# Performance work log

Hardware: AMD Instinct MI355X
Metric: run time of the kernel (lower is better)

## Reference

```python
import jax, jax.numpy as jnp
import numpy as np

HEAD_K_DIM = 128  # linear_key_head_dim (not derivable from weight shapes alone)
EPS_NORM = 1e-6


def _l2norm(x, eps=1e-6):
    return x * jax.lax.rsqrt(jnp.sum(x * x, axis=-1, keepdims=True) + eps)


def setup_inputs() -> dict:
    key = jax.random.key(0)
    ks = jax.random.split(key, 9)
    B, S, H = 2, 1024, 2048
    Hv, Hk, Dk, Dv, K = 32, 16, 128, 128, 4
    key_dim, value_dim = Hk * Dk, Hv * Dv
    C = 2 * key_dim + value_dim  # conv_dim = 8192
    s = 0.02
    return {
        "hidden_states": jax.random.normal(ks[0], (B, S, H), jnp.float32),
        "conv_state": jnp.zeros((B, C, K - 1), jnp.float32),
        "recurrent_state": jnp.zeros((B, Hv, Dk, Dv), jnp.float32),
        "W_qkv": (jax.random.normal(ks[1], (C, H)) * s).astype(jnp.float32),
        "W_z": (jax.random.normal(ks[2], (value_dim, H)) * s).astype(jnp.float32),
        "W_b": (jax.random.normal(ks[3], (Hv, H)) * s).astype(jnp.float32),
        "W_a": (jax.random.normal(ks[4], (Hv, H)) * s).astype(jnp.float32),
        "conv_w": (jax.random.normal(ks[5], (C, K)) * s).astype(jnp.float32),
        "dt_bias": jnp.ones((Hv,), jnp.float32),
        "A_log": jnp.log(jax.random.uniform(ks[6], (Hv,), jnp.float32, 1e-3, 16.0)),
        "norm_weight": jnp.ones((Dv,), jnp.float32),
        "W_out": (jax.random.normal(ks[7], (H, value_dim)) * s).astype(jnp.float32),
    }


def reference(hidden_states, conv_state, recurrent_state, W_qkv, W_z, W_b, W_a,
              conv_w, dt_bias, A_log, norm_weight, W_out):
    B, S, H = hidden_states.shape
    Hv = dt_bias.shape[0]
    Dv = norm_weight.shape[0]
    C, K = conv_w.shape
    value_dim = Hv * Dv
    key_dim = (C - value_dim) // 2
    Dk = HEAD_K_DIM
    Hk = key_dim // Dk

    # input projections
    mixed_qkv = jnp.einsum('bsh,ch->bcs', hidden_states, W_qkv)  # (B, C, S)
    z = hidden_states @ W_z.T                                    # (B, S, value_dim)
    b = hidden_states @ W_b.T                                    # (B, S, Hv)
    a = hidden_states @ W_a.T                                    # (B, S, Hv)

    # causal depthwise conv over time with cached prefix state
    padded = jnp.concatenate([conv_state, mixed_qkv], axis=-1)   # (B, C, K-1+S)
    conv_out = sum(padded[:, :, k:k + S] * conv_w[:, k][None, :, None]
                   for k in range(K))                            # (B, C, S)
    conv_state_new = padded[:, :, -(K - 1):]
    mixed = jnp.swapaxes(jax.nn.silu(conv_out), 1, 2)            # (B, S, C)

    q = mixed[..., :key_dim].reshape(B, S, Hk, Dk)
    k = mixed[..., key_dim:2 * key_dim].reshape(B, S, Hk, Dk)
    v = mixed[..., 2 * key_dim:].reshape(B, S, Hv, Dv)

    beta = jax.nn.sigmoid(b)                                     # (B, S, Hv)
    g = -jnp.exp(A_log) * jax.nn.softplus(a + dt_bias)           # (B, S, Hv)

    rep = Hv // Hk
    if rep > 1:
        q = jnp.repeat(q, rep, axis=2)
        k = jnp.repeat(k, rep, axis=2)

    scale = Dk ** (-0.5)
    q = _l2norm(q) * scale
    k = _l2norm(k)

    # time-leading for scan: (S, B, Hv, ...)
    qT, kT, vT = (jnp.moveaxis(x, 1, 0) for x in (q, k, v))
    gT, betaT = jnp.moveaxis(g, 1, 0), jnp.moveaxis(beta, 1, 0)

    def step(state, xs):
        q_t, k_t, v_t, g_t, beta_t = xs
        state = state * jnp.exp(g_t)[..., None, None]            # decay
        kv_mem = jnp.einsum('bhk,bhkv->bhv', k_t, state)         # read
        delta = (v_t - kv_mem) * beta_t[..., None]               # correction
        state = state + jnp.einsum('bhk,bhv->bhkv', k_t, delta)  # write
        out_t = jnp.einsum('bhk,bhkv->bhv', q_t, state)          # readout
        return state, out_t

    final_state, outs = jax.lax.scan(step, recurrent_state.astype(jnp.float32),
                                     (qT, kT, vT, gT, betaT))
    core = jnp.moveaxis(outs, 0, 1)                              # (B, S, Hv, Dv)

    # gated RMS norm per value head
    var = jnp.mean(core * core, axis=-1, keepdims=True)
    xn = core * jax.lax.rsqrt(var + EPS_NORM) * norm_weight
    gated = xn * jax.nn.silu(z.reshape(B, S, Hv, Dv))

    output = gated.reshape(B, S, value_dim) @ W_out.T            # (B, S, H)
    return output, conv_state_new, final_state
```

## Files before the change

kernel.cpp:

```cpp
#include <hip/hip_runtime.h>
#include <cstdint>
#include <cstddef>

#define B_ 2
#define S_ 1024
#define H_ 2048
#define HV_ 32
#define HK_ 16
#define DK_ 128
#define DV_ 128
#define CC_ 8192
#define KEYDIM_ 2048
#define VALDIM_ 4096
#define NC_ 16
#define CS_ 64
#define NBIG 12416
#define NBIGP 12544

typedef __attribute__((ext_vector_type(8))) short bf16x8;
typedef __attribute__((ext_vector_type(4))) float f32x4;

__device__ __forceinline__ ushort f2bf_rne(float x) {
  union { float f; uint32_t u; } c; c.f = x;
  uint32_t u = c.u + 0x7FFFu + ((c.u >> 16) & 1u);
  return (ushort)(u >> 16);
}

__device__ __forceinline__ void gld16(const void* g, void* l) {
  __builtin_amdgcn_global_load_lds(
      (const __attribute__((address_space(1))) void*)g,
      (__attribute__((address_space(3))) void*)l, 16, 0, 0);
}

__global__ void f2bf_kernel(const float* __restrict__ in, ushort* __restrict__ out, int n) {
  int i = (blockIdx.x * 256 + threadIdx.x) * 4;
  if (i >= n) return;
  float4 v = *(const float4*)(in + i);
  ushort4 o;
  o.x = f2bf_rne(v.x); o.y = f2bf_rne(v.y);
  o.z = f2bf_rne(v.z); o.w = f2bf_rne(v.w);
  *(ushort4*)(out + i) = o;
}

__global__ void wcat_kernel(const float* __restrict__ Wqkv, const float* __restrict__ Wz,
                            const float* __restrict__ Wb, const float* __restrict__ Wa,
                            ushort* __restrict__ out) {
  int i = (blockIdx.x * 256 + threadIdx.x) * 4;
  if (i >= NBIGP * H_) return;
  int n = i >> 11;
  int k = i & (H_ - 1);
  float4 v = make_float4(0.f, 0.f, 0.f, 0.f);
  if (n < 8192)       v = *(const float4*)(Wqkv + (size_t)n * H_ + k);
  else if (n < 12288) v = *(const float4*)(Wz + (size_t)(n - 8192) * H_ + k);
  else if (n < 12320) v = *(const float4*)(Wb + (size_t)(n - 12288) * H_ + k);
  else if (n < 12352) v = *(const float4*)(Wa + (size_t)(n - 12320) * H_ + k);
  ushort4 o;
  o.x = f2bf_rne(v.x); o.y = f2bf_rne(v.y);
  o.z = f2bf_rne(v.z); o.w = f2bf_rne(v.w);
  *(ushort4*)(out + i) = o;
}

#define MEMF() asm volatile("" ::: "memory")
#define VMW(n) asm volatile("s_waitcnt vmcnt(" #n ")" ::: "memory")
#define BARR() do { __builtin_amdgcn_s_barrier(); MEMF(); } while (0)

#define ST(P, SHM, RG, o, kq) do {                                  \
    gld16((P) + (kq),      &SHM[o][((RG) * 2 + 0) * 512]);          \
    gld16((P) + (kq) + 32, &SHM[o][((RG) * 2 + 1) * 512]);          \
  } while (0)

#define LDA(ah, c) do { _Pragma("unroll")                                            \
    for (int i_ = 0; i_ < 4; i_++) { _Pragma("unroll")                               \
      for (int h_ = 0; h_ < 2; h_++)                                                 \
        aF[i_ * 2 + h_] = *(const bf16x8*)(                                          \
            &sAm[c][((wm * 8 + (ah) * 4 + i_) * 2 + h_) * 512 + lane * 8]); } } while (0)

#define LDB(dst, bh, c) do { _Pragma("unroll")                                       \
    for (int j_ = 0; j_ < 2; j_++) { _Pragma("unroll")                               \
      for (int h_ = 0; h_ < 2; h_++)                                                 \
        dst[j_ * 2 + h_] = *(const bf16x8*)(                                         \
            &sBm[c][((wn * 4 + (bh) * 2 + j_) * 2 + h_) * 512 + lane * 8]); } } while (0)

#define MM(ah, bh, bsrc) do {                                                        \
    __builtin_amdgcn_s_setprio(1);                                                   \
    _Pragma("unroll") for (int h_ = 0; h_ < 2; h_++)                                 \
    _Pragma("unroll") for (int i_ = 0; i_ < 4; i_++)                                 \
    _Pragma("unroll") for (int j_ = 0; j_ < 2; j_++)                                 \
      acc[(ah) * 4 + i_][(bh) * 2 + j_] = __builtin_amdgcn_mfma_f32_16x16x32_bf16(   \
          aF[i_ * 2 + h_], bsrc[j_ * 2 + h_], acc[(ah) * 4 + i_][(bh) * 2 + j_],     \
          0, 0, 0);                                                                  \
    __builtin_amdgcn_s_setprio(0);                                                   \
  } while (0)

__global__ __launch_bounds__(512, 2) void gemm256_8ph(
    const ushort* __restrict__ A, const ushort* __restrict__ B,
    float* __restrict__ C, int Ns, int K)
{
  __shared__ ushort sAm[2][16384];
  __shared__ ushort sBm[2][16384];

  const int t = threadIdx.x;
  const int wave = t >> 6, lane = t & 63;
  const int wm = wave >> 2, wn = wave & 3;
  const int l15 = lane & 15, l4 = lane >> 4;
  const int mt = blockIdx.x, nt = blockIdx.y;

  const int rgS0 = (wave & 3) + (wave >> 2) * 8;
  const int rgS3 = rgS0 + 4;
  const int rgS1 = (wave & 1) + (wave >> 1) * 4;
  const int rgS2 = rgS1 + 2;

  const ushort* aP0 = A + (size_t)(mt * 256 + rgS0 * 16 + l15) * K + l4 * 8;
  const ushort* aP1 = A + (size_t)(mt * 256 + rgS3 * 16 + l15) * K + l4 * 8;
  const ushort* bP0 = B + (size_t)(nt * 256 + rgS1 * 16 + l15) * K + l4 * 8;
  const ushort* bP1 = B + (size_t)(nt * 256 + rgS2 * 16 + l15) * K + l4 * 8;

  f32x4 acc[8][4];
  #pragma unroll
  for (int i = 0; i < 8; i++)
    #pragma unroll
    for (int j = 0; j < 4; j++)
      #pragma unroll
      for (int r = 0; r < 4; r++) acc[i][j][r] = 0.f;

  bf16x8 aF[8], bF0[4], bF1[4];

  ST(aP0, sAm, rgS0, 0, 0); MEMF();
  ST(bP0, sBm, rgS1, 0, 0); MEMF();
  ST(bP1, sBm, rgS2, 0, 0); MEMF();
  ST(aP1, sAm, rgS3, 0, 0); MEMF();
  ST(aP0, sAm, rgS0, 1, 64); MEMF();
  VMW(6); BARR();

  const int NT = K >> 6;
  for (int tt = 0; tt < NT; tt++) {
    const int c = tt & 1, o = c ^ 1;
    const int kq1 = (tt + 1 < NT) ? (tt + 1) << 6 : 0;
    const int kq2 = (tt + 2 < NT) ? (tt + 2) << 6 : 0;
    LDA(0, c); LDB(bF0, 0, c);
    VMW(4); BARR();
    ST(bP0, sBm, rgS1, o, kq1); MEMF();
    MM(0, 0, bF0);
    BARR();
    LDB(bF1, 1, c);
    VMW(4); BARR();
    ST(bP1, sBm, rgS2, o, kq1); MEMF();
    MM(0, 1, bF1);
    BARR();
    LDA(1, c);
    VMW(4); BARR();
    ST(aP1, sAm, rgS3, o, kq1); MEMF();
    MM(1, 1, bF1);
    BARR();
    VMW(4); BARR();
    ST(aP0, sAm, rgS0, c, kq2); MEMF();
    MM(1, 0, bF0);
    BARR();
  }
  VMW(0);

  #pragma unroll
  for (int mf = 0; mf < 8; mf++) {
    const int row0 = mt * 256 + wm * 128 + mf * 16 + l4 * 4;
    #pragma unroll
    for (int nf = 0; nf < 4; nf++) {
      const int col = nt * 256 + wn * 64 + nf * 16 + l15;
      if (col < Ns) {
        #pragma unroll
        for (int r = 0; r < 4; r++)
          C[(size_t)(row0 + r) * Ns + col] = acc[mf][nf][r];
      }
    }
  }
}

__device__ __forceinline__ void stage_tile(
    const ushort* aS0, const ushort* aS1, const ushort* bS0, const ushort* bS1,
    ushort* ldsA, ushort* ldsB, int wave, int k0)
{
  #pragma unroll
  for (int h = 0; h < 2; h++) {
    gld16(aS0 + k0 + h * 32, ldsA + h * 4096 + (wave * 2 + 0) * 512);
    gld16(aS1 + k0 + h * 32, ldsA + h * 4096 + (wave * 2 + 1) * 512);
    gld16(bS0 + k0 + h * 32, ldsB + h * 4096 + (wave * 2 + 0) * 512);
    gld16(bS1 + k0 + h * 32, ldsB + h * 4096 + (wave * 2 + 1) * 512);
  }
}

__global__ __launch_bounds__(256) void gemm_bf16_nt(
    const ushort* __restrict__ A, const ushort* __restrict__ B,
    float* __restrict__ C, int M, int N, int K)
{
  __shared__ ushort sL[2][2][8192];
  int t = threadIdx.x;
  int wave = t >> 6, lane = t & 63;
  int wm = wave >> 1, wn = wave & 1;
  int lrow = lane & 15, quad = lane >> 4;
  int mt = blockIdx.x, nt = blockIdx.y;

  f32x4 acc[4][4];
  #pragma unroll
  for (int i = 0; i < 4; i++)
    #pragma unroll
    for (int j = 0; j < 4; j++)
      #pragma unroll
      for (int r = 0; r < 4; r++) acc[i][j][r] = 0.f;

  const ushort* aS0 = A + (size_t)(mt * 128 + (wave * 2 + 0) * 16 + lrow) * K + quad * 8;
  const ushort* aS1 = A + (size_t)(mt * 128 + (wave * 2 + 1) * 16 + lrow) * K + quad * 8;
  const ushort* bS0 = B + (size_t)(nt * 128 + (wave * 2 + 0) * 16 + lrow) * K + quad * 8;
  const ushort* bS1 = B + (size_t)(nt * 128 + (wave * 2 + 1) * 16 + lrow) * K + quad * 8;

  stage_tile(aS0, aS1, bS0, bS1, &sL[0][0][0], &sL[0][1][0], wave, 0);
  __syncthreads();

  const int NK = K >> 6;
  for (int it = 0; it < NK; it++) {
    if (it + 1 < NK)
      stage_tile(aS0, aS1, bS0, bS1,
                 &sL[(it + 1) & 1][0][0], &sL[(it + 1) & 1][1][0],
                 wave, (it + 1) * 64);
    const ushort* bufA = &sL[it & 1][0][0];
    const ushort* bufB = &sL[it & 1][1][0];
    #pragma unroll
    for (int h = 0; h < 2; h++) {
      bf16x8 af[4], bfr[4];
      #pragma unroll
      for (int i = 0; i < 4; i++)
        af[i] = *(const bf16x8*)(bufA + h * 4096 + (wm * 4 + i) * 512 + lane * 8);
      #pragma unroll
      for (int j = 0; j < 4; j++)
        bfr[j] = *(const bf16x8*)(bufB + h * 4096 + (wn * 4 + j) * 512 + lane * 8);
      #pragma unroll
      for (int i = 0; i < 4; i++)
        #pragma unroll
        for (int j = 0; j < 4; j++)
          acc[i][j] = __builtin_amdgcn_mfma_f32_16x16x32_bf16(af[i], bfr[j], acc[i][j], 0, 0, 0);
    }
    __syncthreads();
  }

  #pragma unroll
  for (int i = 0; i < 4; i++) {
    int m_base = mt * 128 + wm * 64 + i * 16 + quad * 4;
    #pragma unroll
    for (int j = 0; j < 4; j++) {
      int n = nt * 128 + wn * 64 + j * 16 + lrow;
      #pragma unroll
      for (int rr = 0; rr < 4; rr++)
        C[(size_t)(m_base + rr) * N + n] = acc[i][j][rr];
    }
  }
}

__global__ void convstate_kernel(const float* __restrict__ Cbig,
                                 float* __restrict__ out)
{
  int idx = blockIdx.x * blockDim.x + threadIdx.x;
  if (idx >= B_ * CC_ * 3) return;
  int j = idx % 3;
  int c = (idx / 3) % CC_;
  int b = idx / (3 * CC_);
  out[idx] = Cbig[((size_t)(b * S_ + (S_ - 3 + j))) * NBIG + c];
}

__global__ __launch_bounds__(128) void prep_qkv(
    const float* __restrict__ Cbig, const float* __restrict__ conv_state,
    const float* __restrict__ conv_w,
    float* __restrict__ Qn, float* __restrict__ Kn, float* __restrict__ Vb)
{
  int group = blockIdx.x, s = blockIdx.y, b = blockIdx.z;
  int t = threadIdx.x;
  int c = group * 128 + t;
  float acc = 0.f;
  #pragma unroll
  for (int kk = 0; kk < 4; kk++) {
    int sp = s - 3 + kk;
    float x = (sp < 0) ? conv_state[((size_t)(b * CC_ + c)) * 3 + (3 + sp)]
                       : Cbig[((size_t)(b * S_ + sp)) * NBIG + c];
    acc += conv_w[c * 4 + kk] * x;
  }
  float val = acc / (1.f + __expf(-acc));

  if (group < 32) {
    __shared__ float red2[2];
    float p = val * val;
    #pragma unroll
    for (int off = 32; off > 0; off >>= 1) p += __shfl_xor(p, off);
    if ((t & 63) == 0) red2[t >> 6] = p;
    __syncthreads();
    float r = rsqrtf(red2[0] + red2[1] + 1e-6f);
    if (group < 16) {
      r *= 0.08838834764831845f;
      Qn[(((size_t)(b * HK_ + group)) * S_ + s) * DK_ + t] = val * r;
    } else {
      Kn[(((size_t)(b * HK_ + (group - 16))) * S_ + s) * DK_ + t] = val * r;
    }
  } else {
    Vb[(((size_t)(b * HV_ + (group - 32))) * S_ + s) * DV_ + t] = val;
  }
}

__global__ void prep_gb(const float* __restrict__ Cbig,
                        const float* __restrict__ A_log, const float* __restrict__ dt_bias,
                        float* __restrict__ g_buf, float* __restrict__ beta_buf)
{
  int idx = blockIdx.x * blockDim.x + threadIdx.x;
  if (idx >= B_ * HV_ * S_) return;
  int s = idx & (S_ - 1);
  int hv = (idx >> 10) & 31;
  int b = idx >> 15;
  float bv = Cbig[((size_t)(b * S_ + s)) * NBIG + 12288 + hv];
  float av = Cbig[((size_t)(b * S_ + s)) * NBIG + 12320 + hv];
  float x = av + dt_bias[hv];
  float sp = (x > 20.f) ? x : log1pf(__expf(x));
  g_buf[idx] = -__expf(A_log[hv]) * sp;
  beta_buf[idx] = 1.f / (1.f + __expf(-bv));
}

__device__ __forceinline__ int swf4(int r, int f) { return r * 32 + (f ^ (r & 31)); }
__device__ __forceinline__ int swf1(int r, int k) {
  return r * 128 + 4 * ((k >> 2) ^ (r & 31)) + (k & 3);
}

__global__ __launch_bounds__(256) void cp_kernel(
    const float* __restrict__ Qn, const float* __restrict__ Kn,
    const float* __restrict__ Vb,
    const float* __restrict__ g_buf, const float* __restrict__ beta_buf,
    float* __restrict__ G_buf, float* __restrict__ M_buf,
    float* __restrict__ KcD, float* __restrict__ D0p)
{
  __shared__ float sK[64 * 128];
  __shared__ float sX[32 * 128];
  __shared__ float sT[64 * 64];
  float* sG  = sT;
  float* sBe = sT + 64;
  float* sA  = sX;
  float* tTw = sX;
  float* tTb = sX;
  float4* sK4 = (float4*)sK;
  float4* sX4 = (float4*)sX;

  const int ch = blockIdx.x;
  const int bh = ch / NC_, c = ch % NC_;
  const int b = bh >> 5, hv = bh & 31, hk = hv >> 1;
  const int s0 = c * CS_;
  const int t = threadIdx.x;
  const size_t gOff = (size_t)bh * S_ + s0;

  float Gw0 = 0.f, Bw0 = 0.f;
  if (t < 64) {
    float gi = g_buf[gOff + t];
    Gw0 = gi;
    #pragma unroll
    for (int off = 1; off < 64; off <<= 1) {
      float o = __shfl_up(Gw0, off);
      if (t >= off) Gw0 += o;
    }
    G_buf[gOff + t] = Gw0;
    sG[t] = Gw0;
    Bw0 = beta_buf[gOff + t];
    sBe[t] = Bw0;
  }
  {
    const float4* src = (const float4*)(Kn + ((size_t)(b * HK_ + hk) * S_ + s0) * DK_);
    #pragma unroll
    for (int u = 0; u < 8; u++) {
      int idx = u * 256 + t;
      sK4[swf4(idx >> 5, idx & 31)] = src[idx];
    }
  }
  __syncthreads();

  const float4* qsrc = (const float4*)(Qn + ((size_t)(b * HK_ + hk) * S_ + s0) * DK_);
  {
    int ti2 = t >> 4, tj = t & 15;
    for (int h = 0; h < 2; h++) {
      #pragma unroll
      for (int u = 0; u < 4; u++) {
        int idx = u * 256 + t;
        sX4[swf4(idx >> 5, idx & 31)] = qsrc[h * 1024 + idx];
      }
      __syncthreads();
      float accM[2][4];
      #pragma unroll
      for (int a = 0; a < 2; a++)
        #pragma unroll
        for (int e = 0; e < 4; e++) accM[a][e] = 0.f;
      for (int k4 = 0; k4 < 32; k4++) {
        float4 qv[2], kv[4];
        qv[0] = sX4[swf4(ti2, k4)];
        qv[1] = sX4[swf4(ti2 + 16, k4)];
        #pragma unroll
        for (int e = 0; e < 4; e++) kv[e] = sK4[swf4(tj + 16 * e, k4)];
        #pragma unroll
        for (int a = 0; a < 2; a++)
          #pragma unroll
          for (int e = 0; e < 4; e++)
            accM[a][e] += qv[a].x * kv[e].x + qv[a].y * kv[e].y +
                          qv[a].z * kv[e].z + qv[a].w * kv[e].w;
      }
      #pragma unroll
      for (int a = 0; a < 2; a++) {
        int iG = h * 32 + ti2 + 16 * a;
        float Gi = sG[iG];
        #pragma unroll
        for (int e = 0; e < 4; e++) {
          int j = tj + 16 * e;
          float m = (j <= iG) ? __expf(Gi - sG[j]) * accM[a][e] : 0.f;
          M_buf[(size_t)ch * 4096 + iG * 64 + j] = m;
        }
      }
      __syncthreads();
    }
  }

  {
    int ti = t >> 4, tj = t & 15;
    float accA[4][4];
    #pragma unroll
    for (int a = 0; a < 4; a++)
      #pragma unroll
      for (int e = 0; e < 4; e++) accA[a][e] = 0.f;
    for (int k4 = 0; k4 < 32; k4++) {
      float4 ki[4], kj[4];
      #pragma unroll
      for (int e = 0; e < 4; e++) {
        ki[e] = sK4[swf4(ti + 16 * e, k4)];
        kj[e] = sK4[swf4(tj + 16 * e, k4)];
      }
      #pragma unroll
      for (int a = 0; a < 4; a++)
        #pragma unroll
        for (int e = 0; e < 4; e++)
          accA[a][e] += ki[a].x * kj[e].x + ki[a].y * kj[e].y +
                        ki[a].z * kj[e].z + ki[a].w * kj[e].w;
    }
    float resA[4][4];
    #pragma unroll
    for (int a = 0; a < 4; a++) {
      int i = ti + 16 * a;
      float Gi = sG[i], Bi = sBe[i];
      #pragma unroll
      for (int e = 0; e < 4; e++) {
        int j = tj + 16 * e;
        resA[a][e] = (j < i) ? Bi * __expf(Gi - sG[j]) * accA[a][e] : 0.f;
      }
    }
    __syncthreads();
    #pragma unroll
    for (int a = 0; a < 4; a++)
      #pragma unroll
      for (int e = 0; e < 4; e++)
        sA[(ti + 16 * a) * 64 + (tj + 16 * e)] = resA[a][e];
  }
  __syncthreads();

  if (t < 64) {
    sT[t] = (t == 0) ? 1.f : 0.f;
    for (int i = 1; i < 64; i++) {
      float acc = 0.f;
      for (int j = 0; j < i; j++) acc += sA[i * 64 + j] * sT[j * 64 + t];
      sT[i * 64 + t] = ((t == i) ? 1.f : 0.f) - acc;
    }
    float w = Bw0 * __expf(Gw0);
    for (int j = 0; j < 64; j++) {
      float wj = __shfl(w, j);
      tTw[j * 64 + t] = sT[t * 64 + j] * wj;
    }
  }
  __syncthreads();

  {
    int i04 = t >> 4, tk = t & 15;
    float accK[4][8];
    #pragma unroll
    for (int r = 0; r < 4; r++)
      #pragma unroll
      for (int u = 0; u < 8; u++) accK[r][u] = 0.f;
    for (int j = 0; j < 64; j++) {
      float4 tw = ((float4*)tTw)[j * 16 + i04];
      #pragma unroll
      for (int u = 0; u < 8; u++) {
        float kv = sK[swf1(j, tk + 16 * u)];
        accK[0][u] += tw.x * kv; accK[1][u] += tw.y * kv;
        accK[2][u] += tw.z * kv; accK[3][u] += tw.w * kv;
      }
    }
    size_t base = (size_t)ch * NBIG;
    #pragma unroll
    for (int r = 0; r < 4; r++)
      #pragma unroll
      for (int u = 0; u < 8; u++)
        KcD[base + (i04 * 4 + r) * 128 + tk + 16 * u] = accK[r][u];
  }
  __syncthreads();

  if (t < 64) {
    for (int j = 0; j < 64; j++) {
      float bj = __shfl(Bw0, j);
      tTb[j * 64 + t] = sT[t * 64 + j] * bj;
    }
  }
  {
    const float4* src = (const float4*)(Vb + ((size_t)bh * S_ + s0) * DV_);
    #pragma unroll
    for (int u = 0; u < 8; u++) {
      int idx = u * 256 + t;
      sK4[swf4(idx >> 5, idx & 31)] = src[idx];
    }
  }
  __syncthreads();

  {
    int i04 = t >> 4, tv_ = t & 15;
    float accD[4][8];
    #pragma unroll
    for (int r = 0; r < 4; r++)
      #pragma unroll
      for (int u = 0; u < 8; u++) accD[r][u] = 0.f;
    for (int j = 0; j < 64; j++) {
      float4 tb = ((float4*)tTb)[j * 16 + i04];
      #pragma unroll
      for (int u = 0; u < 8; u++) {
        float vv = sK[swf1(j, tv_ + 16 * u)];
        accD[0][u] += tb.x * vv; accD[1][u] += tb.y * vv;
        accD[2][u] += tb.z * vv; accD[3][u] += tb.w * vv;
      }
    }
    size_t base = (size_t)ch * NBIG;
    #pragma unroll
    for (int r = 0; r < 4; r++)
      #pragma unroll
      for (int u = 0; u < 8; u++)
        D0p[base + (i04 * 4 + r) * 128 + tv_ + 16 * u] = accD[r][u];
  }
}

__global__ __launch_bounds__(256) void phaseb_kernel(
    const float* __restrict__ rec_state, const float* __restrict__ Qn,
    const float* __restrict__ Kn, const float* __restrict__ G_buf,
    float* __restrict__ KcD, const float* __restrict__ D0p,
    float* __restrict__ Oq_buf, float* __restrict__ final_state)
{
  __shared__ float sS[128 * 32];
  __shared__ float sKT[128 * 64];
  __shared__ float sQT[128 * 64];
  __shared__ float sD[64 * 32];

  const int blk = blockIdx.x;
  const int bh = (blk & 7) | ((blk >> 5) << 3);
  const int vq = (blk >> 3) & 3;
  const int b = bh >> 5, hv = bh & 31, hk = hv >> 1;
  const int t = threadIdx.x;
  const int vbase = vq * 32;
  const float* gG = G_buf + (size_t)bh * S_;

  #pragma unroll
  for (int u = 0; u < 4; u++) {
    int idx = u * 256 + t;
    int k = idx >> 3;
    int v4 = (idx & 7) * 4;
    *(float4*)(&sS[k * 32 + v4]) =
        *(const float4*)(&rec_state[((size_t)bh * 128 + k) * 128 + vbase + v4]);
  }
  __syncthreads();

  const int si = t & 63, skq = t >> 6;
  const int ti = t >> 3;
  const int tv = t & 7;
  const int tk = t >> 3;

  for (int c = 0; c < NC_; c++) {
    const size_t ch = (size_t)bh * NC_ + c;
    const int s0 = c * CS_;
    const float GC = gG[s0 + 63];
    const float eGC = __expf(GC);

    {
      float eGi = __expf(gG[s0 + si]);
      const float* kcRow = KcD + ch * NBIG + si * 128 + skq * 32;
      const float* qRow  = Qn + ((size_t)(b * HK_ + hk) * S_ + s0 + si) * DK_ + skq * 32;
      #pragma unroll
      for (int u = 0; u < 8; u++) {
        float4 kc = *(const float4*)(kcRow + u * 4);
        float4 qv = *(const float4*)(qRow + u * 4);
        int kk = skq * 32 + u * 4;
        sKT[(kk + 0) * 64 + si] = kc.x; sKT[(kk + 1) * 64 + si] = kc.y;
        sKT[(kk + 2) * 64 + si] = kc.z; sKT[(kk + 3) * 64 + si] = kc.w;
        sQT[(kk + 0) * 64 + si] = qv.x * eGi; sQT[(kk + 1) * 64 + si] = qv.y * eGi;
        sQT[(kk + 2) * 64 + si] = qv.z * eGi; sQT[(kk + 3) * 64 + si] = qv.w * eGi;
      }
    }
    __syncthreads();

    {
      float accD[2][4], accO[2][4];
      #pragma unroll
      for (int r = 0; r < 2; r++) {
        float4 d0 = *(const float4*)(&D0p[ch * NBIG + (size_t)(ti * 2 + r) * 128 + vbase + tv * 4]);
        accD[r][0] = d0.x; accD[r][1] = d0.y; accD[r][2] = d0.z; accD[r][3] = d0.w;
        accO[r][0] = accO[r][1] = accO[r][2] = accO[r][3] = 0.f;
      }
      for (int k = 0; k < 128; k++) {
        float2 kc = *(const float2*)(&sKT[k * 64 + ti * 2]);
        float2 qb = *(const float2*)(&sQT[k * 64 + ti * 2]);
        float4 sv = *(const float4*)(&sS[k * 32 + tv * 4]);
        accD[0][0] -= kc.x * sv.x; accD[0][1] -= kc.x * sv.y;
        accD[0][2] -= kc.x * sv.z; accD[0][3] -= kc.x * sv.w;
        accD[1][0] -= kc.y * sv.x; accD[1][1] -= kc.y * sv.y;
        accD[1][2] -= kc.y * sv.z; accD[1][3] -= kc.y * sv.w;
        accO[0][0] += qb.x * sv.x; accO[0][1] += qb.x * sv.y;
        accO[0][2] += qb.x * sv.z; accO[0][3] += qb.x * sv.w;
        accO[1][0] += qb.y * sv.x; accO[1][1] += qb.y * sv.y;
        accO[1][2] += qb.y * sv.z; accO[1][3] += qb.y * sv.w;
      }
      #pragma unroll
      for (int r = 0; r < 2; r++) {
        int i = ti * 2 + r;
        float4 dv = make_float4(accD[r][0], accD[r][1], accD[r][2], accD[r][3]);
        float4 ov = make_float4(accO[r][0], accO[r][1], accO[r][2], accO[r][3]);
        *(float4*)(&sD[i * 32 + tv * 4]) = dv;
        *(float4*)(&KcD[ch * NBIG + (size_t)i * 128 + vbase + tv * 4]) = dv;
        *(float4*)(&Oq_buf[ch * 8192 + (size_t)i * 128 + vbase + tv * 4]) = ov;
      }
    }
    __syncthreads();

    {
      float sc = __expf(GC - gG[s0 + si]);
      const float* kRow = Kn + ((size_t)(b * HK_ + hk) * S_ + s0 + si) * DK_ + skq * 32;
      #pragma unroll
      for (int u = 0; u < 8; u++) {
        float4 x = *(const float4*)(kRow + u * 4);
        x.x *= sc; x.y *= sc; x.z *= sc; x.w *= sc;
        int kg = skq * 8 + u;
        *(float4*)(&sKT[si * 128 + 4 * (kg ^ (si & 31))]) = x;
      }
    }
    __syncthreads();

    {
      float acc[4][4];
      #pragma unroll
      for (int r = 0; r < 4; r++)
        acc[r][0] = acc[r][1] = acc[r][2] = acc[r][3] = 0.f;
      for (int i = 0; i < 64; i++) {
        float4 d  = *(const float4*)(&sD[i * 32 + tv * 4]);
        float4 ka = *(const float4*)(&sKT[i * 128 + 4 * (tk ^ (i & 31))]);
        acc[0][0] += ka.x * d.x; acc[0][1] += ka.x * d.y;
        acc[0][2] += ka.x * d.z; acc[0][3] += ka.x * d.w;
        acc[1][0] += ka.y * d.x; acc[1][1] += ka.y * d.y;
        acc[1][2] += ka.y * d.z; acc[1][3] += ka.y * d.w;
        acc[2][0] += ka.z * d.x; acc[2][1] += ka.z * d.y;
        acc[2][2] += ka.z * d.z; acc[2][3] += ka.z * d.w;
        acc[3][0] += ka.w * d.x; acc[3][1] += ka.w * d.y;
        acc[3][2] += ka.w * d.z; acc[3][3] += ka.w * d.w;
      }
      #pragma unroll
      for (int r = 0; r < 4; r++) {
        int k = tk * 4 + r;
        float4 s = *(const float4*)(&sS[k * 32 + tv * 4]);
        s.x = s.x * eGC + acc[r][0]; s.y = s.y * eGC + acc[r][1];
        s.z = s.z * eGC + acc[r][2]; s.w = s.w * eGC + acc[r][3];
        *(float4*)(&sS[k * 32 + tv * 4]) = s;
      }
    }
    __syncthreads();
  }

  #pragma unroll
  for (int u = 0; u < 4; u++) {
    int idx = u * 256 + t;
    int k = idx >> 3;
    int v4 = (idx & 7) * 4;
    *(float4*)(&final_state[((size_t)bh * 128 + k) * 128 + vbase + v4]) =
        *(const float4*)(&sS[k * 32 + v4]);
  }
}

__global__ __launch_bounds__(128) void phasec_kernel(
    const float* __restrict__ KcD, const float* __restrict__ Oq_buf,
    const float* __restrict__ M_buf, const float* __restrict__ norm_weight,
    const float* __restrict__ Cbig, ushort* __restrict__ zg_bf)
{
  __shared__ float sM[4096];
  __shared__ float red[2][2];
  int ch = blockIdx.x;
  int bh = ch / NC_, c = ch % NC_;
  int b = bh >> 5, hv = bh & 31;
  int s0 = c * CS_;
  int v = threadIdx.x;

  float Dr[64];
  #pragma unroll
  for (int j = 0; j < 64; j++) Dr[j] = KcD[(size_t)ch * NBIG + j * 128 + v];
  {
    const float4* src = (const float4*)(M_buf + (size_t)ch * 4096);
    #pragma unroll
    for (int u = 0; u < 8; u++) ((float4*)sM)[u * 128 + v] = src[u * 128 + v];
  }
  __syncthreads();
  float nw = norm_weight[v];

  for (int i = 0; i < 64; i++) {
    float o = Oq_buf[(size_t)ch * 8192 + i * 128 + v];
    const float4* mr = (const float4*)(sM + i * 64);
    #pragma unroll
    for (int j4 = 0; j4 < 16; j4++) {
      float4 m = mr[j4];
      o += m.x * Dr[4 * j4] + m.y * Dr[4 * j4 + 1] +
           m.z * Dr[4 * j4 + 2] + m.w * Dr[4 * j4 + 3];
    }
    float p = o * o;
    #pragma unroll
    for (int off = 32; off > 0; off >>= 1) p += __shfl_xor(p, off);
    if ((v & 63) == 0) red[i & 1][v >> 6] = p;
    __syncthreads();
    float var = (red[i & 1][0] + red[i & 1][1]) * (1.f / 128.f);
    float xn = o * rsqrtf(var + 1e-6f) * nw;
    float zv = Cbig[((size_t)(b * S_ + s0 + i)) * NBIG + 8192 + hv * DV_ + v];
    zg_bf[((size_t)(b * S_ + s0 + i)) * VALDIM_ + hv * DV_ + v] =
        f2bf_rne(xn * (zv / (1.f + __expf(-zv))));
  }
}

extern "C" void kernel_launch(void* const* d_in, const int* in_sizes, int n_in,
                              void* d_out, int out_size, void* d_ws, size_t ws_size,
                              hipStream_t stream)
{
  const float* hs          = (const float*)d_in[0];
  const float* conv_state  = (const float*)d_in[1];
  const float* rec_state   = (const float*)d_in[2];
  const float* W_qkv       = (const float*)d_in[3];
  const float* W_z         = (const float*)d_in[4];
  const float* W_b         = (const float*)d_in[5];
  const float* W_a         = (const float*)d_in[6];
  const float* conv_w      = (const float*)d_in[7];
  const float* dt_bias     = (const float*)d_in[8];
  const float* A_log       = (const float*)d_in[9];
  const float* norm_weight = (const float*)d_in[10];
  const float* W_out       = (const float*)d_in[11];

  float* out       = (float*)d_out;
  float* out_conv  = out + (size_t)B_ * S_ * H_;
  float* out_state = out_conv + (size_t)B_ * CC_ * 3;

  float* ws = (float*)d_ws;
  float* Cbig = ws;
  float* KcD  = Cbig;
  float* D0p  = Cbig + (size_t)1024 * NBIG;
  float* g_buf    = ws + 25427968;
  float* beta_buf = ws + 25493504;
  float* G_buf    = ws + 25559040;
  float* Qn       = ws + 25624576;
  float* Kn       = ws + 29818880;
  float* Vb       = ws + 34013184;
  float* M_buf    = ws + 42401792;
  float* Oq_buf   = Vb;

  ushort* Wcat_bf = (ushort*)(ws + 25427968);
  ushort* hs_bf   = (ushort*)(ws + 38273024);
  ushort* zg_bf   = (ushort*)Qn;
  ushort* Wout_bf = (ushort*)Kn;

  const int M = B_ * S_;

  f2bf_kernel<<<(M * H_) / 1024, 256, 0, stream>>>(hs, hs_bf, M * H_);
  wcat_kernel<<<(NBIGP * H_) / 1024, 256, 0, stream>>>(W_qkv, W_z, W_b, W_a, Wcat_bf);
  gemm256_8ph<<<dim3(M / 256, NBIGP / 256), 512, 0, stream>>>(hs_bf, Wcat_bf, Cbig, NBIG, H_);
  convstate_kernel<<<(B_ * CC_ * 3 + 255) / 256, 256, 0, stream>>>(Cbig, out_conv);
  prep_qkv<<<dim3(64, S_, B_), 128, 0, stream>>>(Cbig, conv_state, conv_w, Qn, Kn, Vb);
  prep_gb<<<(B_ * HV_ * S_ + 255) / 256, 256, 0, stream>>>(Cbig, A_log, dt_bias, g_buf, beta_buf);
  cp_kernel<<<B_ * HV_ * NC_, 256, 0, stream>>>(Qn, Kn, Vb, g_buf, beta_buf,
                                                G_buf, M_buf, KcD, D0p);
  phaseb_kernel<<<B_ * HV_ * 4, 256, 0, stream>>>(rec_state, Qn, Kn, G_buf,
                                                  KcD, D0p, Oq_buf, out_state);
  f2bf_kernel<<<(H_ * VALDIM_) / 1024, 256, 0, stream>>>(W_out, Wout_bf, H_ * VALDIM_);
  phasec_kernel<<<B_ * HV_ * NC_, 128, 0, stream>>>(KcD, Oq_buf, M_buf,
                                                    norm_weight, Cbig, zg_bf);
  gemm_bf16_nt<<<dim3(M / 128, H_ / 128), 256, 0, stream>>>(zg_bf, Wout_bf, out, M, H_, VALDIM_);
}
```

Baseline: 942.2 us.

## Double phaseb threads with split-K reduction over the recurrent state

Doubles the phase-B block size from 256 to 512 threads. The 128-wide K loop of the chunk output/correction product is split across two thread groups whose partial sums are reduced through a new shared buffer, and the state update gives each thread half as many rows. The sequential scan over chunks runs only 256 blocks, so this aims to shorten per-block latency by adding parallelism per block. The cost is an extra shared-memory reduction and barrier each chunk, more shared memory per block, and idle threads during the reduction.

```diff
diff --git a/kernel.cpp b/kernel.cpp
--- a/kernel.cpp
+++ b/kernel.cpp
@@ -537,7 +537,7 @@
   }
 }
 
-__global__ __launch_bounds__(256) void phaseb_kernel(
+__global__ __launch_bounds__(512) void phaseb_kernel(
     const float* __restrict__ rec_state, const float* __restrict__ Qn,
     const float* __restrict__ Kn, const float* __restrict__ G_buf,
     float* __restrict__ KcD, const float* __restrict__ D0p,
@@ -547,6 +547,7 @@
   __shared__ float sKT[128 * 64];
   __shared__ float sQT[128 * 64];
   __shared__ float sD[64 * 32];
+  __shared__ float sR[2][64 * 32];
 
   const int blk = blockIdx.x;
   const int bh = (blk & 7) | ((blk >> 5) << 3);
@@ -557,8 +558,8 @@
   const float* gG = G_buf + (size_t)bh * S_;
 
   #pragma unroll
-  for (int u = 0; u < 4; u++) {
-    int idx = u * 256 + t;
+  for (int u = 0; u < 2; u++) {
+    int idx = u * 512 + t;
     int k = idx >> 3;
     int v4 = (idx & 7) * 4;
     *(float4*)(&sS[k * 32 + v4]) =
@@ -567,9 +568,10 @@
   __syncthreads();
 
   const int si = t & 63, skq = t >> 6;
-  const int ti = t >> 3;
-  const int tv = t & 7;
-  const int tk = t >> 3;
+  const int kg = t >> 8;
+  const int tt = t & 255;
+  const int ti = tt >> 3, tv = t & 7;
+  const int tp = t >> 3;
 
   for (int c = 0; c < NC_; c++) {
     const size_t ch = (size_t)bh * NC_ + c;
@@ -579,13 +581,13 @@
 
     {
       float eGi = __expf(gG[s0 + si]);
-      const float* kcRow = KcD + ch * NBIG + si * 128 + skq * 32;
-      const float* qRow  = Qn + ((size_t)(b * HK_ + hk) * S_ + s0 + si) * DK_ + skq * 32;
-      #pragma unroll
-      for (int u = 0; u < 8; u++) {
+      const float* kcRow = KcD + ch * NBIG + si * 128 + skq * 16;
+      const float* qRow  = Qn + ((size_t)(b * HK_ + hk) * S_ + s0 + si) * DK_ + skq * 16;
+      #pragma unroll
+      for (int u = 0; u < 4; u++) {
         float4 kc = *(const float4*)(kcRow + u * 4);
         float4 qv = *(const float4*)(qRow + u * 4);
-        int kk = skq * 32 + u * 4;
+        int kk = skq * 16 + u * 4;
         sKT[(kk + 0) * 64 + si] = kc.x; sKT[(kk + 1) * 64 + si] = kc.y;
         sKT[(kk + 2) * 64 + si] = kc.z; sKT[(kk + 3) * 64 + si] = kc.w;
         sQT[(kk + 0) * 64 + si] = qv.x * eGi; sQT[(kk + 1) * 64 + si] = qv.y * eGi;
@@ -598,11 +600,18 @@
       float accD[2][4], accO[2][4];
       #pragma unroll
       for (int r = 0; r < 2; r++) {
-        float4 d0 = *(const float4*)(&D0p[ch * NBIG + (size_t)(ti * 2 + r) * 128 + vbase + tv * 4]);
-        accD[r][0] = d0.x; accD[r][1] = d0.y; accD[r][2] = d0.z; accD[r][3] = d0.w;
         accO[r][0] = accO[r][1] = accO[r][2] = accO[r][3] = 0.f;
-      }
-      for (int k = 0; k < 128; k++) {
+        accD[r][0] = accD[r][1] = accD[r][2] = accD[r][3] = 0.f;
+      }
+      if (kg == 0) {
+        #pragma unroll
+        for (int r = 0; r < 2; r++) {
+          float4 d0 = *(const float4*)(&D0p[ch * NBIG + (size_t)(ti * 2 + r) * 128 + vbase + tv * 4]);
+          accD[r][0] = d0.x; accD[r][1] = d0.y; accD[r][2] = d0.z; accD[r][3] = d0.w;
+        }
+      }
+      const int k0 = kg << 6;
+      for (int k = k0; k < k0 + 64; k++) {
         float2 kc = *(const float2*)(&sKT[k * 64 + ti * 2]);
         float2 qb = *(const float2*)(&sQT[k * 64 + ti * 2]);
         float4 sv = *(const float4*)(&sS[k * 32 + tv * 4]);
@@ -615,51 +624,63 @@
         accO[1][0] += qb.y * sv.x; accO[1][1] += qb.y * sv.y;
         accO[1][2] += qb.y * sv.z; accO[1][3] += qb.y * sv.w;
       }
-      #pragma unroll
-      for (int r = 0; r < 2; r++) {
-        int i = ti * 2 + r;
-        float4 dv = make_float4(accD[r][0], accD[r][1], accD[r][2], accD[r][3]);
-        float4 ov = make_float4(accO[r][0], accO[r][1], accO[r][2], accO[r][3]);
-        *(float4*)(&sD[i * 32 + tv * 4]) = dv;
-        *(float4*)(&KcD[ch * NBIG + (size_t)i * 128 + vbase + tv * 4]) = dv;
-        *(float4*)(&Oq_buf[ch * 8192 + (size_t)i * 128 + vbase + tv * 4]) = ov;
-      }
-    }
-    __syncthreads();
+      if (kg == 1) {
+        #pragma unroll
+        for (int r = 0; r < 2; r++) {
+          int i = ti * 2 + r;
+          *(float4*)(&sR[0][i * 32 + tv * 4]) =
+              make_float4(accD[r][0], accD[r][1], accD[r][2], accD[r][3]);
+          *(float4*)(&sR[1][i * 32 + tv * 4]) =
+              make_float4(accO[r][0], accO[r][1], accO[r][2], accO[r][3]);
+        }
+      }
+      __syncthreads();
+      if (kg == 0) {
+        #pragma unroll
+        for (int r = 0; r < 2; r++) {
+          int i = ti * 2 + r;
+          float4 pD = *(const float4*)(&sR[0][i * 32 + tv * 4]);
+          float4 pO = *(const float4*)(&sR[1][i * 32 + tv * 4]);
+          float4 dv = make_float4(accD[r][0] + pD.x, accD[r][1] + pD.y,
+                                  accD[r][2] + pD.z, accD[r][3] + pD.w);
+          float4 ov = make_float4(accO[r][0] + pO.x, accO[r][1] + pO.y,
+                                  accO[r][2] + pO.z, accO[r][3] + pO.w);
+          *(float4*)(&sD[i * 32 + tv * 4]) = dv;
+          *(float4*)(&KcD[ch * NBIG + (size_t)i * 128 + vbase + tv * 4]) = dv;
+          *(float4*)(&Oq_buf[ch * 8192 + (size_t)i * 128 + vbase + tv * 4]) = ov;
+        }
+      }
+    }
 
     {
       float sc = __expf(GC - gG[s0 + si]);
-      const float* kRow = Kn + ((size_t)(b * HK_ + hk) * S_ + s0 + si) * DK_ + skq * 32;
-      #pragma unroll
-      for (int u = 0; u < 8; u++) {
+      const float* kRow = Kn + ((size_t)(b * HK_ + hk) * S_ + s0 + si) * DK_ + skq * 16;
+      #pragma unroll
+      for (int u = 0; u < 4; u++) {
         float4 x = *(const float4*)(kRow + u * 4);
         x.x *= sc; x.y *= sc; x.z *= sc; x.w *= sc;
-        int kg = skq * 8 + u;
-        *(float4*)(&sKT[si * 128 + 4 * (kg ^ (si & 31))]) = x;
+        int kgr = skq * 4 + u;
+        *(float4*)(&sKT[si * 128 + 4 * (kgr ^ (si & 31))]) = x;
       }
     }
     __syncthreads();
 
     {
-      float acc[4][4];
-      #pragma unroll
-      for (int r = 0; r < 4; r++)
-        acc[r][0] = acc[r][1] = acc[r][2] = acc[r][3] = 0.f;
+      float acc[2][4];
+      acc[0][0] = acc[0][1] = acc[0][2] = acc[0][3] = 0.f;
+      acc[1][0] = acc[1][1] = acc[1][2] = acc[1][3] = 0.f;
+      const int kgr = tp >> 1, kh = (tp & 1) * 2;
       for (int i = 0; i < 64; i++) {
         float4 d  = *(const float4*)(&sD[i * 32 + tv * 4]);
-        float4 ka = *(const float4*)(&sKT[i * 128 + 4 * (tk ^ (i & 31))]);
+        float2 ka = *(const float2*)(&sKT[i * 128 + 4 * (kgr ^ (i & 31)) + kh]);
         acc[0][0] += ka.x * d.x; acc[0][1] += ka.x * d.y;
         acc[0][2] += ka.x * d.z; acc[0][3] += ka.x * d.w;
         acc[1][0] += ka.y * d.x; acc[1][1] += ka.y * d.y;
         acc[1][2] += ka.y * d.z; acc[1][3] += ka.y * d.w;
-        acc[2][0] += ka.z * d.x; acc[2][1] += ka.z * d.y;
-        acc[2][2] += ka.z * d.z; acc[2][3] += ka.z * d.w;
-        acc[3][0] += ka.w * d.x; acc[3][1] += ka.w * d.y;
-        acc[3][2] += ka.w * d.z; acc[3][3] += ka.w * d.w;
-      }
-      #pragma unroll
-      for (int r = 0; r < 4; r++) {
-        int k = tk * 4 + r;
+      }
+      #pragma unroll
+      for (int r = 0; r < 2; r++) {
+        int k = tp * 2 + r;
         float4 s = *(const float4*)(&sS[k * 32 + tv * 4]);
         s.x = s.x * eGC + acc[r][0]; s.y = s.y * eGC + acc[r][1];
         s.z = s.z * eGC + acc[r][2]; s.w = s.w * eGC + acc[r][3];
@@ -670,8 +691,8 @@
   }
 
   #pragma unroll
-  for (int u = 0; u < 4; u++) {
-    int idx = u * 256 + t;
+  for (int u = 0; u < 2; u++) {
+    int idx = u * 512 + t;
     int k = idx >> 3;
     int v4 = (idx & 7) * 4;
     *(float4*)(&final_state[((size_t)bh * 128 + k) * 128 + vbase + v4]) =
@@ -774,7 +795,7 @@
   prep_gb<<<(B_ * HV_ * S_ + 255) / 256, 256, 0, stream>>>(Cbig, A_log, dt_bias, g_buf, beta_buf);
   cp_kernel<<<B_ * HV_ * NC_, 256, 0, stream>>>(Qn, Kn, Vb, g_buf, beta_buf,
                                                 G_buf, M_buf, KcD, D0p);
-  phaseb_kernel<<<B_ * HV_ * 4, 256, 0, stream>>>(rec_state, Qn, Kn, G_buf,
+  phaseb_kernel<<<B_ * HV_ * 4, 512, 0, stream>>>(rec_state, Qn, Kn, G_buf,
                                                   KcD, D0p, Oq_buf, out_state);
   f2bf_kernel<<<(H_ * VALDIM_) / 1024, 256, 0, stream>>>(W_out, Wout_bf, H_ * VALDIM_);
   phasec_kernel<<<B_ * HV_ * NC_, 128, 0, stream>>>(KcD, Oq_buf, M_buf,
```

New measurement: 916.7 us. 2.7% less time.
